# Performance work log

Hardware: AMD Instinct MI355X
Metric: run time of the kernel (lower is better)

The kernel has to match this reference:

```python
import jax, jax.numpy as jnp
import numpy as np

DIM = 256
HEADS = 8
HEAD_DIM = DIM // HEADS  # 32
LN_EPS = 1e-5


def setup_inputs() -> dict:
    key = jax.random.key(0)
    ks = jax.random.split(key, 11)
    B, N = 8, 4096
    s = 1.0 / np.sqrt(DIM)
    return {
        "q": jax.random.normal(ks[0], (B, N, DIM), dtype=jnp.float32),
        "k": jax.random.normal(ks[1], (B, N, DIM), dtype=jnp.float32),
        "v": jax.random.normal(ks[2], (B, N, DIM), dtype=jnp.float32),
        "Wq": jax.random.normal(ks[3], (DIM, DIM), dtype=jnp.float32) * s,
        "bq": jax.random.normal(ks[4], (DIM,), dtype=jnp.float32) * 0.01,
        "Wk": jax.random.normal(ks[5], (DIM, DIM), dtype=jnp.float32) * s,
        "bk": jax.random.normal(ks[6], (DIM,), dtype=jnp.float32) * 0.01,
        "Wv": jax.random.normal(ks[7], (DIM, DIM), dtype=jnp.float32) * s,
        "bv": jax.random.normal(ks[8], (DIM,), dtype=jnp.float32) * 0.01,
        "ln_gamma": jnp.ones((DIM,), dtype=jnp.float32),
        "ln_beta": jnp.zeros((DIM,), dtype=jnp.float32),
    }


def _heads(x, B, N):
    # [B, N, DIM] -> [B, HEADS, N, HEAD_DIM]
    return x.reshape(B, N, HEADS, HEAD_DIM).transpose(0, 2, 1, 3)


def reference(q, k, v, Wq, bq, Wk, bk, Wv, bv, ln_gamma, ln_beta):
    B, N, _ = q.shape
    ql = _heads(q @ Wq.T + bq, B, N)
    kl = _heads(k @ Wk.T + bk, B, N)
    vl = _heads(v @ Wv.T + bv, B, N)

    # FFT-domain "attention": rfft2 over (seq, head_dim), complex multiply, irfft2
    q_fft = jnp.fft.rfft2(ql.astype(jnp.float32))   # [B, H, N, HEAD_DIM//2+1] complex
    k_fft = jnp.fft.rfft2(kl.astype(jnp.float32))
    attention = jnp.fft.irfft2(q_fft * k_fft)        # [B, H, N, HEAD_DIM]
    attention = jax.nn.softmax(attention, axis=-1)

    out = vl * attention                             # elementwise value gate
    out = out.transpose(0, 2, 1, 3).reshape(B, N, HEADS * HEAD_DIM)

    # dropout is identity at eval; residual + LayerNorm(256)
    out = out + v
    mu = jnp.mean(out, axis=-1, keepdims=True)
    var = jnp.var(out, axis=-1, keepdims=True)
    out = (out - mu) * jax.lax.rsqrt(var + LN_EPS) * ln_gamma + ln_beta
    return out
```

## Files before the change

kernel.cpp:

```cpp
#include <hip/hip_runtime.h>

#define NFREQ 2049

using cf = float2;
typedef __attribute__((ext_vector_type(8))) short short8;
typedef __attribute__((ext_vector_type(4))) float floatx4;

__device__ inline unsigned short bf16_rne(float x) {
  unsigned u = __float_as_uint(x);
  unsigned r = u + 0x7FFFu + ((u >> 16) & 1u);
  return (unsigned short)(r >> 16);
}
__device__ inline float bf16_to_f(unsigned short h) {
  return __uint_as_float(((unsigned)h) << 16);
}

__global__ __launch_bounds__(256, 4) void gemm_proj(
    const float* __restrict__ X, const float* __restrict__ W,
    const float* __restrict__ bias, float* __restrict__ dst, int mode)
{
  __shared__ __align__(16) unsigned short sm[12416];
  unsigned short* sAhi = sm;
  unsigned short* sAlo = sm + 4128;
  unsigned short* sBhi = sm + 8256;
  unsigned short* sBlo = sm + 10336;

  const int tid = threadIdx.x;
  const int m0 = blockIdx.x * 128;
  const int j0 = blockIdx.y * 64;
  const int wave = tid >> 6, lane = tid & 63;
  const int wm = wave & 1, wj = wave >> 1;
  const int lm = lane & 15, quad = lane >> 4;

  floatx4 acc[4][2] = {};

  for (int k0 = 0; k0 < 256; k0 += 32) {
    float4 xa[4], wb[2];
    #pragma unroll
    for (int r = 0; r < 4; r++) {
      int v = tid + r * 256;
      int row = v >> 3, c4 = (v & 7) * 4;
      xa[r] = *(const float4*)(X + (size_t)(m0 + row) * 256 + k0 + c4);
    }
    #pragma unroll
    for (int r = 0; r < 2; r++) {
      int v = tid + r * 256;
      int row = v >> 3, c4 = (v & 7) * 4;
      wb[r] = *(const float4*)(W + (size_t)(j0 + row) * 256 + k0 + c4);
    }
    __syncthreads();
    #pragma unroll
    for (int r = 0; r < 4; r++) {
      int v = tid + r * 256;
      int row = v >> 3, c4 = (v & 7) * 4;
      int q = c4 >> 3, off = c4 & 7;
      float f[4] = {xa[r].x, xa[r].y, xa[r].z, xa[r].w};
      unsigned short h[4], l[4];
      #pragma unroll
      for (int i = 0; i < 4; i++) {
        h[i] = bf16_rne(f[i]);
        l[i] = bf16_rne(f[i] - bf16_to_f(h[i]));
      }
      int idx = ((q * 129 + row) << 3) + off;
      *(uint2*)&sAhi[idx] = make_uint2((unsigned)h[0] | ((unsigned)h[1] << 16),
                                       (unsigned)h[2] | ((unsigned)h[3] << 16));
      *(uint2*)&sAlo[idx] = make_uint2((unsigned)l[0] | ((unsigned)l[1] << 16),
                                       (unsigned)l[2] | ((unsigned)l[3] << 16));
    }
    #pragma unroll
    for (int r = 0; r < 2; r++) {
      int v = tid + r * 256;
      int row = v >> 3, c4 = (v & 7) * 4;
      int q = c4 >> 3, off = c4 & 7;
      float f[4] = {wb[r].x, wb[r].y, wb[r].z, wb[r].w};
      unsigned short h[4], l[4];
      #pragma unroll
      for (int i = 0; i < 4; i++) {
        h[i] = bf16_rne(f[i]);
        l[i] = bf16_rne(f[i] - bf16_to_f(h[i]));
      }
      int idx = ((q * 65 + row) << 3) + off;
      *(uint2*)&sBhi[idx] = make_uint2((unsigned)h[0] | ((unsigned)h[1] << 16),
                                       (unsigned)h[2] | ((unsigned)h[3] << 16));
      *(uint2*)&sBlo[idx] = make_uint2((unsigned)l[0] | ((unsigned)l[1] << 16),
                                       (unsigned)l[2] | ((unsigned)l[3] << 16));
    }
    __syncthreads();

    short8 ahi[4], alo[4], bhi[2], blo[2];
    #pragma unroll
    for (int mf = 0; mf < 4; mf++) {
      int row = wm * 64 + mf * 16 + lm;
      int idx = ((quad * 129 + row) << 3);
      ahi[mf] = *(const short8*)&sAhi[idx];
      alo[mf] = *(const short8*)&sAlo[idx];
    }
    #pragma unroll
    for (int jf = 0; jf < 2; jf++) {
      int row = wj * 32 + jf * 16 + lm;
      int idx = ((quad * 65 + row) << 3);
      bhi[jf] = *(const short8*)&sBhi[idx];
      blo[jf] = *(const short8*)&sBlo[idx];
    }
    #pragma unroll
    for (int mf = 0; mf < 4; mf++)
      #pragma unroll
      for (int jf = 0; jf < 2; jf++) {
        acc[mf][jf] = __builtin_amdgcn_mfma_f32_16x16x32_bf16(
            ahi[mf], bhi[jf], acc[mf][jf], 0, 0, 0);
        acc[mf][jf] = __builtin_amdgcn_mfma_f32_16x16x32_bf16(
            ahi[mf], blo[jf], acc[mf][jf], 0, 0, 0);
        acc[mf][jf] = __builtin_amdgcn_mfma_f32_16x16x32_bf16(
            alo[mf], bhi[jf], acc[mf][jf], 0, 0, 0);
      }
  }

  #pragma unroll
  for (int jf = 0; jf < 2; jf++) {
    float bj = bias[j0 + wj * 32 + jf * 16 + lm];
    #pragma unroll
    for (int mf = 0; mf < 4; mf++)
      #pragma unroll
      for (int r = 0; r < 4; r++)
        acc[mf][jf][r] += bj;
  }

  if (mode == 2) {
    #pragma unroll
    for (int mf = 0; mf < 4; mf++)
      #pragma unroll
      for (int jf = 0; jf < 2; jf++) {
        int j = j0 + wj * 32 + jf * 16 + lm;
        int mb = m0 + wm * 64 + mf * 16 + quad * 4;
        #pragma unroll
        for (int r = 0; r < 4; r++)
          dst[(size_t)(mb + r) * 256 + j] = acc[mf][jf][r];
      }
  } else {
    const int b = m0 >> 12;
    const int n0 = m0 & 4095;
    #pragma unroll
    for (int mf = 0; mf < 4; mf++)
      #pragma unroll
      for (int jf = 0; jf < 2; jf++) {
        int j = j0 + wj * 32 + jf * 16 + lm;
        int nb = n0 + wm * 64 + mf * 16 + quad * 4;
        float4 o = make_float4(acc[mf][jf][0], acc[mf][jf][1],
                               acc[mf][jf][2], acc[mf][jf][3]);
        *(float4*)(dst + (size_t)(b * 256 + j) * 4096 + nb) = o;
      }
  }
}

#define FFT_LDS 4368

__device__ inline int swz(int i) { return i + (i >> 4) + (i >> 8); }
__device__ inline int digrev4(int n) {
  int b = __brev((unsigned)n) >> 20;
  return ((b & 0x555) << 1) | ((b & 0xAAA) >> 1);
}

template<int SIGN>
__device__ inline void fft4_stages(cf* X, int tid)
{
  #pragma unroll
  for (int s = 0; s < 6; s++) {
    const int q = 1 << (2 * s);
    __syncthreads();
    #pragma unroll
    for (int r = 0; r < 4; r++) {
      int t = tid + r * 256;
      int j = t & (q - 1);
      int base = ((t >> (2 * s)) << (2 * s + 2)) + j;
      cf a = X[swz(base)];
      cf b = X[swz(base + q)];
      cf c = X[swz(base + 2 * q)];
      cf d = X[swz(base + 3 * q)];
      float th = (float)SIGN * 6.283185307179586f * (float)j / (float)(4 * q);
      float s1, c1, s2, c2, s3, c3;
      __sincosf(th, &s1, &c1);
      __sincosf(2.0f * th, &s2, &c2);
      __sincosf(3.0f * th, &s3, &c3);
      cf bt = make_float2(c1 * b.x - s1 * b.y, c1 * b.y + s1 * b.x);
      cf ct = make_float2(c2 * c.x - s2 * c.y, c2 * c.y + s2 * c.x);
      cf dt = make_float2(c3 * d.x - s3 * d.y, c3 * d.y + s3 * d.x);
      cf e0 = make_float2(a.x + ct.x, a.y + ct.y);
      cf e1 = make_float2(a.x - ct.x, a.y - ct.y);
      cf o0 = make_float2(bt.x + dt.x, bt.y + dt.y);
      cf o1 = make_float2(bt.x - dt.x, bt.y - dt.y);
      cf io1 = make_float2(-o1.y, o1.x);
      X[swz(base)]         = make_float2(e0.x + o0.x, e0.y + o0.y);
      X[swz(base + 2 * q)] = make_float2(e0.x - o0.x, e0.y - o0.y);
      if (SIGN < 0) {
        X[swz(base + q)]     = make_float2(e1.x - io1.x, e1.y - io1.y);
        X[swz(base + 3 * q)] = make_float2(e1.x + io1.x, e1.y + io1.y);
      } else {
        X[swz(base + q)]     = make_float2(e1.x + io1.x, e1.y + io1.y);
        X[swz(base + 3 * q)] = make_float2(e1.x - io1.x, e1.y - io1.y);
      }
    }
  }
  __syncthreads();
}

__global__ __launch_bounds__(256) void fft_fwd(
    const float* __restrict__ src_base, cf* __restrict__ dst_base)
{
  __shared__ cf X[FFT_LDS];
  const int c0 = blockIdx.x * 2;
  const float* s0 = src_base + (size_t)c0 * 4096;
  const float* s1 = s0 + 4096;
  const int tid = threadIdx.x;
  #pragma unroll
  for (int i = 0; i < 16; i++) {
    int n = tid + i * 256;
    X[swz(digrev4(n))] = make_float2(s0[n], s1[n]);
  }
  fft4_stages<-1>(X, tid);
  cf* d0 = dst_base + (size_t)c0 * NFREQ;
  cf* d1 = d0 + NFREQ;
  for (int f = tid; f <= 2048; f += 256) {
    cf Zf = X[swz(f)];
    cf Zm = X[swz((4096 - f) & 4095)];
    d0[f] = make_float2(0.5f * (Zf.x + Zm.x), 0.5f * (Zf.y - Zm.y));
    d1[f] = make_float2(0.5f * (Zf.y + Zm.y), 0.5f * (Zm.x - Zf.x));
  }
}

__device__ inline cf cmul(cf a, cf b) {
  return make_float2(a.x * b.x - a.y * b.y, a.x * b.y + a.y * b.x);
}

__device__ inline cf tw_f(int l, int h) {
  int j = l & (h - 1);
  if (l & h) {
    float sn, cs;
    __sincosf(-3.14159265358979f * (float)j / (float)h, &sn, &cs);
    return make_float2(cs, sn);
  }
  return make_float2(1.0f, 0.0f);
}

template<int H>
__device__ inline cf fwd_stage(cf x, cf w, float sg) {
  float px = __shfl_xor(x.x, H);
  float py = __shfl_xor(x.y, H);
  return cmul(make_float2(px + sg * x.x, py + sg * x.y), w);
}
template<int H>
__device__ inline cf inv_stage(cf x, cf w, float sg) {
  cf t = cmul(x, w);
  float px = __shfl_xor(t.x, H);
  float py = __shfl_xor(t.y, H);
  return make_float2(px + sg * t.x, py + sg * t.y);
}
template<int H>
__device__ inline cf nt_stage(cf x, float sg) {
  float px = __shfl_xor(x.x, H);
  float py = __shfl_xor(x.y, H);
  return make_float2(px + sg * x.x, py + sg * x.y);
}

__global__ __launch_bounds__(256) void freq_conv(
    cf* __restrict__ Qf, const cf* __restrict__ Kf)
{
  __shared__ cf Qs[32][65];
  __shared__ cf Ks[32][65];
  const int f0 = blockIdx.x * 64;
  const int bh = blockIdx.y;
  const int tid = threadIdx.x;
  const int wave = tid >> 6, lane = tid & 63;
  const int d = lane & 31, hl = lane >> 5;

  #pragma unroll
  for (int i = 0; i < 8; i++) {
    int v = tid + i * 256;
    int e = v >> 6, fl = v & 63;
    int f = f0 + fl;
    if (f < NFREQ) {
      Qs[e][fl] = Qf[(size_t)(bh * 32 + e) * NFREQ + f];
      Ks[e][fl] = Kf[(size_t)(bh * 32 + e) * NFREQ + f];
    } else {
      Qs[e][fl] = make_float2(0.0f, 0.0f);
      Ks[e][fl] = make_float2(0.0f, 0.0f);
    }
  }
  __syncthreads();

  const cf w16 = tw_f(d, 16), w8 = tw_f(d, 8), w4 = tw_f(d, 4), w2 = tw_f(d, 2);
  const float s16 = (d & 16) ? -1.0f : 1.0f;
  const float s8  = (d & 8)  ? -1.0f : 1.0f;
  const float s4  = (d & 4)  ? -1.0f : 1.0f;
  const float s2  = (d & 2)  ? -1.0f : 1.0f;
  const float s1  = (d & 1)  ? -1.0f : 1.0f;

  #pragma unroll
  for (int it = 0; it < 8; it++) {
    const int fl = it * 8 + wave * 2 + hl;
    cf q = Qs[d][fl];
    cf k = Ks[d][fl];
    q = fwd_stage<16>(q, w16, s16);  k = fwd_stage<16>(k, w16, s16);
    q = fwd_stage<8>(q, w8, s8);     k = fwd_stage<8>(k, w8, s8);
    q = fwd_stage<4>(q, w4, s4);     k = fwd_stage<4>(k, w4, s4);
    q = fwd_stage<2>(q, w2, s2);     k = fwd_stage<2>(k, w2, s2);
    q = nt_stage<1>(q, s1);          k = nt_stage<1>(k, s1);
    cf c = cmul(q, k);
    c = nt_stage<1>(c, s1);
    c = inv_stage<2>(c, make_float2(w2.x, -w2.y), s2);
    c = inv_stage<4>(c, make_float2(w4.x, -w4.y), s4);
    c = inv_stage<8>(c, make_float2(w8.x, -w8.y), s8);
    c = inv_stage<16>(c, make_float2(w16.x, -w16.y), s16);
    Qs[d][fl] = make_float2(c.x * (1.0f / 32.0f), c.y * (1.0f / 32.0f));
  }
  __syncthreads();

  #pragma unroll
  for (int i = 0; i < 8; i++) {
    int v = tid + i * 256;
    int e = v >> 6, fl = v & 63;
    int f = f0 + fl;
    if (f < NFREQ)
      Qf[(size_t)(bh * 32 + e) * NFREQ + f] = Qs[e][fl];
  }
}

__global__ __launch_bounds__(256) void fft_inv(
    const cf* __restrict__ Cf, float* __restrict__ attn)
{
  __shared__ cf X[FFT_LDS];
  const int c0 = blockIdx.x * 2;
  const cf* s0 = Cf + (size_t)c0 * NFREQ;
  const cf* s1 = s0 + NFREQ;
  const int tid = threadIdx.x;
  for (int f = tid; f <= 2048; f += 256) {
    cf c1 = s0[f];
    cf c2 = s1[f];
    X[swz(digrev4(f))] = make_float2(c1.x - c2.y, c1.y + c2.x);
    if (f != 0 && f != 2048)
      X[swz(digrev4(4096 - f))] = make_float2(c1.x + c2.y, c2.x - c1.y);
  }
  fft4_stages<+1>(X, tid);
  float* d0 = attn + (size_t)c0 * 4096;
  float* d1 = d0 + 4096;
  const float inv = 1.0f / 4096.0f;
  #pragma unroll
  for (int i = 0; i < 16; i++) {
    int n = tid + i * 256;
    cf z = X[swz(n)];
    d0[n] = z.x * inv;
    d1[n] = z.y * inv;
  }
}

__global__ __launch_bounds__(256) void finalize_kernel(
    const float* __restrict__ attn, const float* __restrict__ VL,
    const float* __restrict__ vin, const float* __restrict__ gamma,
    const float* __restrict__ beta, float* __restrict__ out)
{
  __shared__ float At[256][33];
  const int n0 = blockIdx.x * 32;
  const int b = blockIdx.y;
  const int tid = threadIdx.x;
  #pragma unroll
  for (int i = 0; i < 32; i++) {
    int v = tid + i * 256;
    int hd = v >> 5, nn = v & 31;
    At[hd][nn] = attn[(size_t)(b * 256 + hd) * 4096 + n0 + nn];
  }
  __syncthreads();
  const int wave = tid >> 6, lane = tid & 63;
  float g[4], bt[4];
  #pragma unroll
  for (int r = 0; r < 4; r++) { g[r] = gamma[64 * r + lane]; bt[r] = beta[64 * r + lane]; }

  for (int t = 0; t < 8; t++) {
    const int nn = wave * 8 + t;
    const int n = n0 + nn;
    float p[4];
    #pragma unroll
    for (int r = 0; r < 4; r++) {
      float a = At[64 * r + lane][nn];
      float mx = a;
      #pragma unroll
      for (int off = 16; off >= 1; off >>= 1) mx = fmaxf(mx, __shfl_xor(mx, off, 32));
      float e = __expf(a - mx);
      float s = e;
      #pragma unroll
      for (int off = 16; off >= 1; off >>= 1) s += __shfl_xor(s, off, 32);
      p[r] = e / s;
    }
    const size_t base = ((size_t)b * 4096 + n) * 256 + lane;
    float o[4];
    float s1 = 0.0f, s2 = 0.0f;
    #pragma unroll
    for (int r = 0; r < 4; r++) {
      o[r] = VL[base + 64 * r] * p[r] + vin[base + 64 * r];
      s1 += o[r];
      s2 += o[r] * o[r];
    }
    #pragma unroll
    for (int off = 32; off >= 1; off >>= 1) {
      s1 += __shfl_xor(s1, off, 64);
      s2 += __shfl_xor(s2, off, 64);
    }
    float mu = s1 * (1.0f / 256.0f);
    float var = s2 * (1.0f / 256.0f) - mu * mu;
    float rs = rsqrtf(var + 1e-5f);
    #pragma unroll
    for (int r = 0; r < 4; r++)
      out[base + 64 * r] = (o[r] - mu) * rs * g[r] + bt[r];
  }
}

extern "C" void kernel_launch(void* const* d_in, const int* in_sizes, int n_in,
                              void* d_out, int out_size, void* d_ws, size_t ws_size,
                              hipStream_t stream)
{
  const float* q  = (const float*)d_in[0];
  const float* k  = (const float*)d_in[1];
  const float* v  = (const float*)d_in[2];
  const float* Wq = (const float*)d_in[3];
  const float* bq = (const float*)d_in[4];
  const float* Wk = (const float*)d_in[5];
  const float* bk = (const float*)d_in[6];
  const float* Wv = (const float*)d_in[7];
  const float* bv = (const float*)d_in[8];
  const float* ln_gamma = (const float*)d_in[9];
  const float* ln_beta  = (const float*)d_in[10];
  float* out = (float*)d_out;

  float* ws = (float*)d_ws;
  float* QL = ws;
  float* KL = QL + (size_t)8388608;
  float* VL = KL + (size_t)8388608;
  cf* Qf = (cf*)(VL + (size_t)8388608);
  cf* Kf = Qf + (size_t)2048 * NFREQ;
  float* attn = QL;

  gemm_proj<<<dim3(256, 4), 256, 0, stream>>>(q, Wq, bq, QL, 0);
  gemm_proj<<<dim3(256, 4), 256, 0, stream>>>(k, Wk, bk, KL, 1);
  gemm_proj<<<dim3(256, 4), 256, 0, stream>>>(v, Wv, bv, VL, 2);

  fft_fwd<<<1024, 256, 0, stream>>>(QL, Qf);
  fft_fwd<<<1024, 256, 0, stream>>>(KL, Kf);

  freq_conv<<<dim3(33, 64), 256, 0, stream>>>(Qf, Kf);

  fft_inv<<<1024, 256, 0, stream>>>(Qf, attn);

  finalize_kernel<<<dim3(128, 8), 256, 0, stream>>>(attn, VL, v, ln_gamma,
                                                    ln_beta, out);
}
```

Baseline: 325.1 us.

## Switch seq FFT to radix-8 stages and batch projection/FFT launches

Replaces the radix-4 six-stage shared-memory FFT with a radix-8 four-stage FFT. Each butterfly computes one sincos and builds the remaining twiddles by repeated complex multiplication, and the swizzle and digit reversal are adjusted to match. This cuts barriers and LDS passes, at the cost of higher register pressure and slightly more accumulated twiddle error. It also merges the three projection GEMMs into one 3D-grid launch and the two forward FFTs into one 2D-grid launch to cut launch overhead and fill the GPU better.

```diff
diff --git a/kernel.cpp b/kernel.cpp
--- a/kernel.cpp
+++ b/kernel.cpp
@@ -14,11 +14,24 @@
 __device__ inline float bf16_to_f(unsigned short h) {
   return __uint_as_float(((unsigned)h) << 16);
 }
+__device__ inline cf cmul(cf a, cf b) {
+  return make_float2(a.x * b.x - a.y * b.y, a.x * b.y + a.y * b.x);
+}
+__device__ inline cf cadd(cf a, cf b) { return make_float2(a.x + b.x, a.y + b.y); }
+__device__ inline cf csub(cf a, cf b) { return make_float2(a.x - b.x, a.y - b.y); }
 
 __global__ __launch_bounds__(256, 4) void gemm_proj(
-    const float* __restrict__ X, const float* __restrict__ W,
-    const float* __restrict__ bias, float* __restrict__ dst, int mode)
-{
+    const float* __restrict__ Xq, const float* __restrict__ Wq, const float* __restrict__ bq,
+    const float* __restrict__ Xk, const float* __restrict__ Wk, const float* __restrict__ bk,
+    const float* __restrict__ Xv, const float* __restrict__ Wv, const float* __restrict__ bv,
+    float* __restrict__ dq, float* __restrict__ dk, float* __restrict__ dv)
+{
+  const int z = blockIdx.z;
+  const float* X = (z == 0) ? Xq : (z == 1) ? Xk : Xv;
+  const float* W = (z == 0) ? Wq : (z == 1) ? Wk : Wv;
+  const float* bias = (z == 0) ? bq : (z == 1) ? bk : bv;
+  float* dst = (z == 0) ? dq : (z == 1) ? dk : dv;
+
   __shared__ __align__(16) unsigned short sm[12416];
   unsigned short* sAhi = sm;
   unsigned short* sAlo = sm + 4128;
@@ -125,7 +138,7 @@
         acc[mf][jf][r] += bj;
   }
 
-  if (mode == 2) {
+  if (z == 2) {
     #pragma unroll
     for (int mf = 0; mf < 4; mf++)
       #pragma unroll
@@ -152,61 +165,79 @@
   }
 }
 
-#define FFT_LDS 4368
-
-__device__ inline int swz(int i) { return i + (i >> 4) + (i >> 8); }
-__device__ inline int digrev4(int n) {
-  int b = __brev((unsigned)n) >> 20;
-  return ((b & 0x555) << 1) | ((b & 0xAAA) >> 1);
+#define FFT_LDS 4376
+
+__device__ inline int swz(int i) { return i + (i >> 4) + (i >> 8) + (i >> 9); }
+__device__ inline int digrev8(int n) {
+  return ((n & 7) << 9) | (((n >> 3) & 7) << 6) | (((n >> 6) & 7) << 3) | ((n >> 9) & 7);
 }
 
 template<int SIGN>
-__device__ inline void fft4_stages(cf* X, int tid)
-{
-  #pragma unroll
-  for (int s = 0; s < 6; s++) {
-    const int q = 1 << (2 * s);
+__device__ inline void fft8_stages(cf* X, int tid)
+{
+  const float C = 0.70710678118654752f;
+  const float sg = (float)SIGN;
+  #pragma unroll
+  for (int s = 0; s < 4; s++) {
+    const int q = 1 << (3 * s);
     __syncthreads();
     #pragma unroll
-    for (int r = 0; r < 4; r++) {
+    for (int r = 0; r < 2; r++) {
       int t = tid + r * 256;
       int j = t & (q - 1);
-      int base = ((t >> (2 * s)) << (2 * s + 2)) + j;
-      cf a = X[swz(base)];
-      cf b = X[swz(base + q)];
-      cf c = X[swz(base + 2 * q)];
-      cf d = X[swz(base + 3 * q)];
-      float th = (float)SIGN * 6.283185307179586f * (float)j / (float)(4 * q);
-      float s1, c1, s2, c2, s3, c3;
-      __sincosf(th, &s1, &c1);
-      __sincosf(2.0f * th, &s2, &c2);
-      __sincosf(3.0f * th, &s3, &c3);
-      cf bt = make_float2(c1 * b.x - s1 * b.y, c1 * b.y + s1 * b.x);
-      cf ct = make_float2(c2 * c.x - s2 * c.y, c2 * c.y + s2 * c.x);
-      cf dt = make_float2(c3 * d.x - s3 * d.y, c3 * d.y + s3 * d.x);
-      cf e0 = make_float2(a.x + ct.x, a.y + ct.y);
-      cf e1 = make_float2(a.x - ct.x, a.y - ct.y);
-      cf o0 = make_float2(bt.x + dt.x, bt.y + dt.y);
-      cf o1 = make_float2(bt.x - dt.x, bt.y - dt.y);
-      cf io1 = make_float2(-o1.y, o1.x);
-      X[swz(base)]         = make_float2(e0.x + o0.x, e0.y + o0.y);
-      X[swz(base + 2 * q)] = make_float2(e0.x - o0.x, e0.y - o0.y);
-      if (SIGN < 0) {
-        X[swz(base + q)]     = make_float2(e1.x - io1.x, e1.y - io1.y);
-        X[swz(base + 3 * q)] = make_float2(e1.x + io1.x, e1.y + io1.y);
-      } else {
-        X[swz(base + q)]     = make_float2(e1.x + io1.x, e1.y + io1.y);
-        X[swz(base + 3 * q)] = make_float2(e1.x - io1.x, e1.y - io1.y);
-      }
+      int base = ((t >> (3 * s)) << (3 * s + 3)) + j;
+      cf x[8];
+      #pragma unroll
+      for (int l = 0; l < 8; l++) x[l] = X[swz(base + l * q)];
+      if (s > 0) {
+        float a = sg * 6.283185307179586f * (float)j / (float)(8 * q);
+        float sn, cs;
+        __sincosf(a, &sn, &cs);
+        cf w1 = make_float2(cs, sn);
+        cf w = w1;
+        #pragma unroll
+        for (int l = 1; l < 8; l++) {
+          x[l] = cmul(x[l], w);
+          if (l < 7) w = cmul(w, w1);
+        }
+      }
+      cf u0 = cadd(x[0], x[4]), v0 = csub(x[0], x[4]);
+      cf u1 = cadd(x[1], x[5]), v1 = csub(x[1], x[5]);
+      cf u2 = cadd(x[2], x[6]), v2 = csub(x[2], x[6]);
+      cf u3 = cadd(x[3], x[7]), v3 = csub(x[3], x[7]);
+      cf w1v = make_float2(C * (v1.x - sg * v1.y), C * (v1.y + sg * v1.x));
+      cf w2v = make_float2(-sg * v2.y, sg * v2.x);
+      cf w3v = make_float2(C * (-v3.x - sg * v3.y), C * (sg * v3.x - v3.y));
+      cf e0 = cadd(u0, u2), e1 = csub(u0, u2);
+      cf o0 = cadd(u1, u3), o1 = csub(u1, u3);
+      cf F0 = cadd(e0, o0), F4 = csub(e0, o0);
+      cf F2 = make_float2(e1.x - sg * o1.y, e1.y + sg * o1.x);
+      cf F6 = make_float2(e1.x + sg * o1.y, e1.y - sg * o1.x);
+      cf e0b = cadd(v0, w2v), e1b = csub(v0, w2v);
+      cf o0b = cadd(w1v, w3v), o1b = csub(w1v, w3v);
+      cf F1 = cadd(e0b, o0b), F5 = csub(e0b, o0b);
+      cf F3 = make_float2(e1b.x - sg * o1b.y, e1b.y + sg * o1b.x);
+      cf F7 = make_float2(e1b.x + sg * o1b.y, e1b.y - sg * o1b.x);
+      X[swz(base + 0 * q)] = F0;
+      X[swz(base + 1 * q)] = F1;
+      X[swz(base + 2 * q)] = F2;
+      X[swz(base + 3 * q)] = F3;
+      X[swz(base + 4 * q)] = F4;
+      X[swz(base + 5 * q)] = F5;
+      X[swz(base + 6 * q)] = F6;
+      X[swz(base + 7 * q)] = F7;
     }
   }
   __syncthreads();
 }
 
 __global__ __launch_bounds__(256) void fft_fwd(
-    const float* __restrict__ src_base, cf* __restrict__ dst_base)
+    const float* __restrict__ srcQ, cf* __restrict__ dstQ,
+    const float* __restrict__ srcK, cf* __restrict__ dstK)
 {
   __shared__ cf X[FFT_LDS];
+  const float* src_base = blockIdx.y ? srcK : srcQ;
+  cf* dst_base = blockIdx.y ? dstK : dstQ;
   const int c0 = blockIdx.x * 2;
   const float* s0 = src_base + (size_t)c0 * 4096;
   const float* s1 = s0 + 4096;
@@ -214,9 +245,9 @@
   #pragma unroll
   for (int i = 0; i < 16; i++) {
     int n = tid + i * 256;
-    X[swz(digrev4(n))] = make_float2(s0[n], s1[n]);
-  }
-  fft4_stages<-1>(X, tid);
+    X[swz(digrev8(n))] = make_float2(s0[n], s1[n]);
+  }
+  fft8_stages<-1>(X, tid);
   cf* d0 = dst_base + (size_t)c0 * NFREQ;
   cf* d1 = d0 + NFREQ;
   for (int f = tid; f <= 2048; f += 256) {
@@ -225,10 +256,6 @@
     d0[f] = make_float2(0.5f * (Zf.x + Zm.x), 0.5f * (Zf.y - Zm.y));
     d1[f] = make_float2(0.5f * (Zf.y + Zm.y), 0.5f * (Zm.x - Zf.x));
   }
-}
-
-__device__ inline cf cmul(cf a, cf b) {
-  return make_float2(a.x * b.x - a.y * b.y, a.x * b.y + a.y * b.x);
 }
 
 __device__ inline cf tw_f(int l, int h) {
@@ -335,11 +362,11 @@
   for (int f = tid; f <= 2048; f += 256) {
     cf c1 = s0[f];
     cf c2 = s1[f];
-    X[swz(digrev4(f))] = make_float2(c1.x - c2.y, c1.y + c2.x);
+    X[swz(digrev8(f))] = make_float2(c1.x - c2.y, c1.y + c2.x);
     if (f != 0 && f != 2048)
-      X[swz(digrev4(4096 - f))] = make_float2(c1.x + c2.y, c2.x - c1.y);
-  }
-  fft4_stages<+1>(X, tid);
+      X[swz(digrev8(4096 - f))] = make_float2(c1.x + c2.y, c2.x - c1.y);
+  }
+  fft8_stages<+1>(X, tid);
   float* d0 = attn + (size_t)c0 * 4096;
   float* d1 = d0 + 4096;
   const float inv = 1.0f / 4096.0f;
@@ -437,12 +464,10 @@
   cf* Kf = Qf + (size_t)2048 * NFREQ;
   float* attn = QL;
 
-  gemm_proj<<<dim3(256, 4), 256, 0, stream>>>(q, Wq, bq, QL, 0);
-  gemm_proj<<<dim3(256, 4), 256, 0, stream>>>(k, Wk, bk, KL, 1);
-  gemm_proj<<<dim3(256, 4), 256, 0, stream>>>(v, Wv, bv, VL, 2);
-
-  fft_fwd<<<1024, 256, 0, stream>>>(QL, Qf);
-  fft_fwd<<<1024, 256, 0, stream>>>(KL, Kf);
+  gemm_proj<<<dim3(256, 4, 3), 256, 0, stream>>>(q, Wq, bq, k, Wk, bk, v, Wv, bv,
+                                                 QL, KL, VL);
+
+  fft_fwd<<<dim3(1024, 2), 256, 0, stream>>>(QL, Qf, KL, Kf);
 
   freq_conv<<<dim3(33, 64), 256, 0, stream>>>(Qf, Kf);
 
```

After: 293.8 us. -9.6%, faster.
